# Kernel tuning notes

Measured on AMD Instinct MI355X. Metric: run time of the kernel, lower is better.

## Reference

```python
import jax, jax.numpy as jnp
import numpy as np


def setup_inputs() -> dict:
    key = jax.random.key(0)
    ks = jax.random.split(key, 5)
    B, N, D = 32, 128, 4096
    return {
        "curr_head": jax.random.normal(ks[0], (B, D), jnp.float32),
        "curr_errors": jax.random.normal(ks[1], (B, N, D), jnp.float32),
        "curr_head_2": jax.random.normal(ks[2], (B, D), jnp.float32),
        "curr_errors_2": jax.random.normal(ks[3], (B, N, D), jnp.float32),
        "adv_errors": jax.random.normal(ks[4], (B, N, D), jnp.float32),
        "shared_errors": 128,
    }


def reference(curr_head, curr_errors, curr_head_2, curr_errors_2, adv_errors, shared_errors):
    B = curr_head.shape[0]
    tail = curr_head.shape[1:]
    # (B, N, *tail) -> (N, B, *tail), matching torch's view + transpose(1, 0)
    e1 = jnp.moveaxis(curr_errors.reshape(B, -1, *tail), 1, 0)
    e2 = jnp.moveaxis(curr_errors_2.reshape(B, -1, *tail), 1, 0)
    N1, N2 = e1.shape[0], e2.shape[0]
    s = int(shared_errors)

    def zeros(n):
        return jnp.zeros((n, B) + tail, e1.dtype)

    # self_errors / factor_errors: (N1 + N2 - s, B, *tail)
    self_errors = jnp.concatenate([e1, zeros(N2 - s)], axis=0)
    factor_errors = jnp.concatenate([e2[:s], zeros(N1 - s), e2[s:]], axis=0)

    lin_err = curr_head[None] * factor_errors + curr_head_2[None] * self_errors
    quadr_const = self_errors * factor_errors

    # Exact identity: 0.5*sum_ij |a_i a_j + a_j a_i| = (sum_i |a_i|)^2 (elementwise),
    # since a_i*a_j is already symmetric. Avoids the (N,N,B,*tail) outer product.
    abs_sum = jnp.abs(self_errors).sum(axis=0)
    quadr_error = abs_sum * abs_sum - 0.5 * jnp.abs(quadr_const).sum(axis=0)

    new_head = curr_head * curr_head_2 + 0.5 * quadr_const.sum(axis=0)

    errors = jnp.moveaxis(lin_err, 0, 1)  # (B, N1+N2-s, *tail)
    new_errors = jnp.concatenate([errors, quadr_error[:, None] * adv_errors], axis=1)
    new_errors = new_errors.reshape(-1, *tail)
    return new_head, new_errors
```

## Files before the change

### kernel.cpp

```cpp
#include <hip/hip_runtime.h>

constexpr int B  = 32;
constexpr int N  = 128;
constexpr int D  = 4096;
constexpr int DV = D / 4;
constexpr int COLS   = 64;
constexpr int CHUNKS = 16;
constexpr int NPC    = N / CHUNKS;
constexpr int TPB    = COLS * CHUNKS;
constexpr int TILES  = DV / COLS;

__device__ __forceinline__ float4 f4add(float4 a, float4 b) {
    return make_float4(a.x + b.x, a.y + b.y, a.z + b.z, a.w + b.w);
}

__global__ __launch_bounds__(TPB) void relaxed_prod_kernel(
    const float* __restrict__ h1,
    const float* __restrict__ e1,
    const float* __restrict__ h2,
    const float* __restrict__ e2,
    const float* __restrict__ adv,
    float* __restrict__ out)
{
    const int lane  = threadIdx.x & (COLS - 1);
    const int chunk = threadIdx.x / COLS;
    const int tile  = blockIdx.x % TILES;
    const int b     = blockIdx.x / TILES;
    const int col   = tile * COLS + lane;
    const long d0   = (long)col * 4;

    const float4* e1p  = (const float4*)(e1  + (long)b * N * D + d0);
    const float4* e2p  = (const float4*)(e2  + (long)b * N * D + d0);
    const float4* advp = (const float4*)(adv + (long)b * N * D + d0);
    float4* lin_out = (float4*)(out + (long)B * D + (long)b * (2 * N) * D + d0);
    float4* adv_out = lin_out + (long)N * DV;

    const float4 vh1 = *(const float4*)(h1 + (long)b * D + d0);
    const float4 vh2 = *(const float4*)(h2 + (long)b * D + d0);

    float4 sq  = make_float4(0.f, 0.f, 0.f, 0.f);
    float4 sa  = make_float4(0.f, 0.f, 0.f, 0.f);
    float4 saq = make_float4(0.f, 0.f, 0.f, 0.f);

    const int n0 = chunk * NPC;
#pragma unroll
    for (int i = 0; i < NPC; ++i) {
        const long off = (long)(n0 + i) * DV;
        float4 a = e1p[off];
        float4 c = e2p[off];
        float4 lin;
        lin.x = vh1.x * c.x + vh2.x * a.x;
        lin.y = vh1.y * c.y + vh2.y * a.y;
        lin.z = vh1.z * c.z + vh2.z * a.z;
        lin.w = vh1.w * c.w + vh2.w * a.w;
        lin_out[off] = lin;
        float4 q = make_float4(a.x * c.x, a.y * c.y, a.z * c.z, a.w * c.w);
        sq  = f4add(sq, q);
        sa.x += fabsf(a.x); sa.y += fabsf(a.y); sa.z += fabsf(a.z); sa.w += fabsf(a.w);
        saq.x += fabsf(q.x); saq.y += fabsf(q.y); saq.z += fabsf(q.z); saq.w += fabsf(q.w);
    }

    __shared__ float4 s_q [CHUNKS][COLS];
    __shared__ float4 s_a [CHUNKS][COLS];
    __shared__ float4 s_aq[CHUNKS][COLS];
    __shared__ float4 s_qe[COLS];
    s_q [chunk][lane] = sq;
    s_a [chunk][lane] = sa;
    s_aq[chunk][lane] = saq;
    __syncthreads();

    if (chunk == 0) {
        float4 tq  = s_q [0][lane];
        float4 ta  = s_a [0][lane];
        float4 taq = s_aq[0][lane];
#pragma unroll
        for (int c = 1; c < CHUNKS; ++c) {
            tq  = f4add(tq,  s_q [c][lane]);
            ta  = f4add(ta,  s_a [c][lane]);
            taq = f4add(taq, s_aq[c][lane]);
        }
        float4 qe;
        qe.x = ta.x * ta.x - 0.5f * taq.x;
        qe.y = ta.y * ta.y - 0.5f * taq.y;
        qe.z = ta.z * ta.z - 0.5f * taq.z;
        qe.w = ta.w * ta.w - 0.5f * taq.w;
        float4 nh;
        nh.x = vh1.x * vh2.x + 0.5f * tq.x;
        nh.y = vh1.y * vh2.y + 0.5f * tq.y;
        nh.z = vh1.z * vh2.z + 0.5f * tq.z;
        nh.w = vh1.w * vh2.w + 0.5f * tq.w;
        *(float4*)(out + (long)b * D + d0) = nh;
        s_qe[lane] = qe;
    }
    __syncthreads();

    const float4 qe = s_qe[lane];
#pragma unroll
    for (int i = 0; i < NPC; ++i) {
        const long off = (long)(n0 + i) * DV;
        float4 v = advp[off];
        float4 r = make_float4(qe.x * v.x, qe.y * v.y, qe.z * v.z, qe.w * v.w);
        adv_out[off] = r;
    }
}

extern "C" void kernel_launch(void* const* d_in, const int* in_sizes, int n_in,
                              void* d_out, int out_size, void* d_ws, size_t ws_size,
                              hipStream_t stream) {
    const float* h1  = (const float*)d_in[0];
    const float* e1  = (const float*)d_in[1];
    const float* h2  = (const float*)d_in[2];
    const float* e2  = (const float*)d_in[3];
    const float* adv = (const float*)d_in[4];
    float* out = (float*)d_out;

    dim3 grid(B * TILES);
    dim3 block(TPB);
    relaxed_prod_kernel<<<grid, block, 0, stream>>>(h1, e1, h2, e2, adv, out);
}
```

Baseline: 288.7 us.

## Split fused kernel into three-stage pipeline with global workspace reduction

Replaces the single fused kernel with three launches. The first streams e1/e2 per batch slab and writes partial sums to the workspace, the second reduces the partials to produce new_head and qe, and the third scales adv by qe. Each thread now owns a full 4096-wide row, and rows are split into slabs across blocks. The aim is to drop the intra-block shared-memory barrier and to give longer contiguous streams per block. The cost is extra kernel launches, workspace traffic, and only B*8=256 blocks in the main kernels. The old fused kernel is kept as a fallback when the workspace is too small.

```diff
diff --git a/kernel.cpp b/kernel.cpp
--- a/kernel.cpp
+++ b/kernel.cpp
@@ -4,117 +4,217 @@
 constexpr int N  = 128;
 constexpr int D  = 4096;
 constexpr int DV = D / 4;
-constexpr int COLS   = 64;
-constexpr int CHUNKS = 16;
-constexpr int NPC    = N / CHUNKS;
-constexpr int TPB    = COLS * CHUNKS;
-constexpr int TILES  = DV / COLS;
 
 __device__ __forceinline__ float4 f4add(float4 a, float4 b) {
     return make_float4(a.x + b.x, a.y + b.y, a.z + b.z, a.w + b.w);
 }
-
-__global__ __launch_bounds__(TPB) void relaxed_prod_kernel(
-    const float* __restrict__ h1,
-    const float* __restrict__ e1,
-    const float* __restrict__ h2,
-    const float* __restrict__ e2,
-    const float* __restrict__ adv,
-    float* __restrict__ out)
-{
-    const int lane  = threadIdx.x & (COLS - 1);
-    const int chunk = threadIdx.x / COLS;
-    const int tile  = blockIdx.x % TILES;
-    const int b     = blockIdx.x / TILES;
-    const int col   = tile * COLS + lane;
-    const long d0   = (long)col * 4;
+__device__ __forceinline__ float4 f4mul(float4 a, float4 b) {
+    return make_float4(a.x * b.x, a.y * b.y, a.z * b.z, a.w * b.w);
+}
+__device__ __forceinline__ float4 f4abs(float4 a) {
+    return make_float4(fabsf(a.x), fabsf(a.y), fabsf(a.z), fabsf(a.w));
+}
+
+template <int SLABS>
+__global__ __launch_bounds__(1024) void k_lin_partial(
+    const float4* __restrict__ h1, const float4* __restrict__ e1,
+    const float4* __restrict__ h2, const float4* __restrict__ e2,
+    float4* __restrict__ out, float4* __restrict__ ws)
+{
+    constexpr int R = N / SLABS;
+    const int c    = threadIdx.x;
+    const int slab = blockIdx.x % SLABS;
+    const int b    = blockIdx.x / SLABS;
+    const int n0   = slab * R;
+
+    const float4* e1p = e1 + ((long)b * N + n0) * DV + c;
+    const float4* e2p = e2 + ((long)b * N + n0) * DV + c;
+    float4* linp = out + (long)B * DV + ((long)b * 2 * N + n0) * DV + c;
+
+    const float4 vh1 = h1[(long)b * DV + c];
+    const float4 vh2 = h2[(long)b * DV + c];
+
+    float4 sq  = make_float4(0.f, 0.f, 0.f, 0.f);
+    float4 sa  = make_float4(0.f, 0.f, 0.f, 0.f);
+    float4 saq = make_float4(0.f, 0.f, 0.f, 0.f);
+
+#pragma unroll 4
+    for (int i = 0; i < R; ++i) {
+        float4 a = e1p[(long)i * DV];
+        float4 f = e2p[(long)i * DV];
+        float4 lin;
+        lin.x = vh1.x * f.x + vh2.x * a.x;
+        lin.y = vh1.y * f.y + vh2.y * a.y;
+        lin.z = vh1.z * f.z + vh2.z * a.z;
+        lin.w = vh1.w * f.w + vh2.w * a.w;
+        linp[(long)i * DV] = lin;
+        float4 q = f4mul(a, f);
+        sq  = f4add(sq, q);
+        sa  = f4add(sa, f4abs(a));
+        saq = f4add(saq, f4abs(q));
+    }
+
+    const long pbase = ((long)b * SLABS + slab) * DV + c;
+    const long asz   = (long)B * SLABS * DV;
+    ws[pbase]           = sq;
+    ws[asz + pbase]     = sa;
+    ws[2 * asz + pbase] = saq;
+}
+
+__global__ __launch_bounds__(256) void k_finalize(
+    const float4* __restrict__ h1, const float4* __restrict__ h2,
+    float4* __restrict__ out, float4* __restrict__ ws, int slabs)
+{
+    const int id = blockIdx.x * 256 + threadIdx.x;
+    const int b  = id / DV;
+    const int c  = id % DV;
+    const long asz = (long)B * slabs * DV;
+
+    float4 tq  = make_float4(0.f, 0.f, 0.f, 0.f);
+    float4 ta  = make_float4(0.f, 0.f, 0.f, 0.f);
+    float4 taq = make_float4(0.f, 0.f, 0.f, 0.f);
+    for (int s = 0; s < slabs; ++s) {
+        const long p = ((long)b * slabs + s) * DV + c;
+        tq  = f4add(tq,  ws[p]);
+        ta  = f4add(ta,  ws[asz + p]);
+        taq = f4add(taq, ws[2 * asz + p]);
+    }
+    const float4 vh1 = h1[id];
+    const float4 vh2 = h2[id];
+    float4 nh, qe;
+    nh.x = vh1.x * vh2.x + 0.5f * tq.x;
+    nh.y = vh1.y * vh2.y + 0.5f * tq.y;
+    nh.z = vh1.z * vh2.z + 0.5f * tq.z;
+    nh.w = vh1.w * vh2.w + 0.5f * tq.w;
+    qe.x = ta.x * ta.x - 0.5f * taq.x;
+    qe.y = ta.y * ta.y - 0.5f * taq.y;
+    qe.z = ta.z * ta.z - 0.5f * taq.z;
+    qe.w = ta.w * ta.w - 0.5f * taq.w;
+    out[id] = nh;
+    ws[3 * asz + id] = qe;
+}
+
+template <int SLABS>
+__global__ __launch_bounds__(1024) void k_adv(
+    const float4* __restrict__ adv, float4* __restrict__ out,
+    const float4* __restrict__ ws)
+{
+    constexpr int R = N / SLABS;
+    const int c    = threadIdx.x;
+    const int slab = blockIdx.x % SLABS;
+    const int b    = blockIdx.x / SLABS;
+    const int n0   = slab * R;
+
+    const float4 qe = ws[3L * B * SLABS * DV + (long)b * DV + c];
+    const float4* ap = adv + ((long)b * N + n0) * DV + c;
+    float4* op = out + (long)B * DV + ((long)b * 2 * N + N + n0) * DV + c;
+
+#pragma unroll 4
+    for (int i = 0; i < R; ++i) {
+        float4 v = ap[(long)i * DV];
+        op[(long)i * DV] = f4mul(qe, v);
+    }
+}
+
+constexpr int FB_COLS = 64, FB_CHUNKS = 16, FB_NPC = N / FB_CHUNKS,
+              FB_TPB = FB_COLS * FB_CHUNKS, FB_TILES = DV / FB_COLS;
+
+__global__ __launch_bounds__(FB_TPB) void relaxed_prod_fallback(
+    const float* __restrict__ h1, const float* __restrict__ e1,
+    const float* __restrict__ h2, const float* __restrict__ e2,
+    const float* __restrict__ adv, float* __restrict__ out)
+{
+    const int lane  = threadIdx.x & (FB_COLS - 1);
+    const int chunk = threadIdx.x / FB_COLS;
+    const int tile  = blockIdx.x % FB_TILES;
+    const int b     = blockIdx.x / FB_TILES;
+    const long d0   = ((long)tile * FB_COLS + lane) * 4;
 
     const float4* e1p  = (const float4*)(e1  + (long)b * N * D + d0);
     const float4* e2p  = (const float4*)(e2  + (long)b * N * D + d0);
     const float4* advp = (const float4*)(adv + (long)b * N * D + d0);
     float4* lin_out = (float4*)(out + (long)B * D + (long)b * (2 * N) * D + d0);
     float4* adv_out = lin_out + (long)N * DV;
-
     const float4 vh1 = *(const float4*)(h1 + (long)b * D + d0);
     const float4 vh2 = *(const float4*)(h2 + (long)b * D + d0);
 
-    float4 sq  = make_float4(0.f, 0.f, 0.f, 0.f);
-    float4 sa  = make_float4(0.f, 0.f, 0.f, 0.f);
-    float4 saq = make_float4(0.f, 0.f, 0.f, 0.f);
-
-    const int n0 = chunk * NPC;
+    float4 sq = make_float4(0,0,0,0), sa = make_float4(0,0,0,0), saq = make_float4(0,0,0,0);
+    const int n0 = chunk * FB_NPC;
 #pragma unroll
-    for (int i = 0; i < NPC; ++i) {
+    for (int i = 0; i < FB_NPC; ++i) {
         const long off = (long)(n0 + i) * DV;
-        float4 a = e1p[off];
-        float4 c = e2p[off];
+        float4 a = e1p[off], f = e2p[off];
         float4 lin;
-        lin.x = vh1.x * c.x + vh2.x * a.x;
-        lin.y = vh1.y * c.y + vh2.y * a.y;
-        lin.z = vh1.z * c.z + vh2.z * a.z;
-        lin.w = vh1.w * c.w + vh2.w * a.w;
+        lin.x = vh1.x * f.x + vh2.x * a.x; lin.y = vh1.y * f.y + vh2.y * a.y;
+        lin.z = vh1.z * f.z + vh2.z * a.z; lin.w = vh1.w * f.w + vh2.w * a.w;
         lin_out[off] = lin;
-        float4 q = make_float4(a.x * c.x, a.y * c.y, a.z * c.z, a.w * c.w);
-        sq  = f4add(sq, q);
-        sa.x += fabsf(a.x); sa.y += fabsf(a.y); sa.z += fabsf(a.z); sa.w += fabsf(a.w);
-        saq.x += fabsf(q.x); saq.y += fabsf(q.y); saq.z += fabsf(q.z); saq.w += fabsf(q.w);
-    }
-
-    __shared__ float4 s_q [CHUNKS][COLS];
-    __shared__ float4 s_a [CHUNKS][COLS];
-    __shared__ float4 s_aq[CHUNKS][COLS];
-    __shared__ float4 s_qe[COLS];
-    s_q [chunk][lane] = sq;
-    s_a [chunk][lane] = sa;
-    s_aq[chunk][lane] = saq;
+        float4 q = f4mul(a, f);
+        sq = f4add(sq, q); sa = f4add(sa, f4abs(a)); saq = f4add(saq, f4abs(q));
+    }
+    __shared__ float4 s_q[FB_CHUNKS][FB_COLS], s_a[FB_CHUNKS][FB_COLS],
+                      s_aq[FB_CHUNKS][FB_COLS], s_qe[FB_COLS];
+    s_q[chunk][lane] = sq; s_a[chunk][lane] = sa; s_aq[chunk][lane] = saq;
     __syncthreads();
-
     if (chunk == 0) {
-        float4 tq  = s_q [0][lane];
-        float4 ta  = s_a [0][lane];
-        float4 taq = s_aq[0][lane];
+        float4 tq = s_q[0][lane], ta = s_a[0][lane], taq = s_aq[0][lane];
 #pragma unroll
-        for (int c = 1; c < CHUNKS; ++c) {
-            tq  = f4add(tq,  s_q [c][lane]);
-            ta  = f4add(ta,  s_a [c][lane]);
-            taq = f4add(taq, s_aq[c][lane]);
+        for (int cc = 1; cc < FB_CHUNKS; ++cc) {
+            tq = f4add(tq, s_q[cc][lane]); ta = f4add(ta, s_a[cc][lane]);
+            taq = f4add(taq, s_aq[cc][lane]);
         }
-        float4 qe;
-        qe.x = ta.x * ta.x - 0.5f * taq.x;
-        qe.y = ta.y * ta.y - 0.5f * taq.y;
-        qe.z = ta.z * ta.z - 0.5f * taq.z;
-        qe.w = ta.w * ta.w - 0.5f * taq.w;
-        float4 nh;
-        nh.x = vh1.x * vh2.x + 0.5f * tq.x;
-        nh.y = vh1.y * vh2.y + 0.5f * tq.y;
-        nh.z = vh1.z * vh2.z + 0.5f * tq.z;
-        nh.w = vh1.w * vh2.w + 0.5f * tq.w;
+        float4 qe, nh;
+        qe.x = ta.x * ta.x - 0.5f * taq.x; qe.y = ta.y * ta.y - 0.5f * taq.y;
+        qe.z = ta.z * ta.z - 0.5f * taq.z; qe.w = ta.w * ta.w - 0.5f * taq.w;
+        nh.x = vh1.x * vh2.x + 0.5f * tq.x; nh.y = vh1.y * vh2.y + 0.5f * tq.y;
+        nh.z = vh1.z * vh2.z + 0.5f * tq.z; nh.w = vh1.w * vh2.w + 0.5f * tq.w;
         *(float4*)(out + (long)b * D + d0) = nh;
         s_qe[lane] = qe;
     }
     __syncthreads();
-
     const float4 qe = s_qe[lane];
 #pragma unroll
-    for (int i = 0; i < NPC; ++i) {
+    for (int i = 0; i < FB_NPC; ++i) {
         const long off = (long)(n0 + i) * DV;
-        float4 v = advp[off];
-        float4 r = make_float4(qe.x * v.x, qe.y * v.y, qe.z * v.z, qe.w * v.w);
-        adv_out[off] = r;
-    }
+        adv_out[off] = f4mul(qe, advp[off]);
+    }
+}
+
+template <int SLABS>
+static void launch_pipeline(const float4* h1, const float4* e1,
+                            const float4* h2, const float4* e2,
+                            const float4* adv, float4* out, float4* ws,
+                            hipStream_t stream)
+{
+    k_lin_partial<SLABS><<<dim3(B * SLABS), dim3(1024), 0, stream>>>(h1, e1, h2, e2, out, ws);
+    k_finalize<<<dim3(B * DV / 256), dim3(256), 0, stream>>>(h1, h2, out, ws, SLABS);
+    k_adv<SLABS><<<dim3(B * SLABS), dim3(1024), 0, stream>>>(adv, out, ws);
 }
 
 extern "C" void kernel_launch(void* const* d_in, const int* in_sizes, int n_in,
                               void* d_out, int out_size, void* d_ws, size_t ws_size,
                               hipStream_t stream) {
-    const float* h1  = (const float*)d_in[0];
-    const float* e1  = (const float*)d_in[1];
-    const float* h2  = (const float*)d_in[2];
-    const float* e2  = (const float*)d_in[3];
-    const float* adv = (const float*)d_in[4];
-    float* out = (float*)d_out;
-
-    dim3 grid(B * TILES);
-    dim3 block(TPB);
-    relaxed_prod_kernel<<<grid, block, 0, stream>>>(h1, e1, h2, e2, adv, out);
-}
+    const float4* h1  = (const float4*)d_in[0];
+    const float4* e1  = (const float4*)d_in[1];
+    const float4* h2  = (const float4*)d_in[2];
+    const float4* e2  = (const float4*)d_in[3];
+    const float4* adv = (const float4*)d_in[4];
+    float4* out = (float4*)d_out;
+    float4* ws  = (float4*)d_ws;
+
+    auto need = [](int slabs) -> size_t {
+        return ((size_t)3 * B * slabs * DV + (size_t)B * DV) * sizeof(float4);
+    };
+    if (ws_size >= need(8)) {
+        launch_pipeline<8>(h1, e1, h2, e2, adv, out, ws, stream);
+    } else if (ws_size >= need(4)) {
+        launch_pipeline<4>(h1, e1, h2, e2, adv, out, ws, stream);
+    } else if (ws_size >= need(2)) {
+        launch_pipeline<2>(h1, e1, h2, e2, adv, out, ws, stream);
+    } else if (ws_size >= need(1)) {
+        launch_pipeline<1>(h1, e1, h2, e2, adv, out, ws, stream);
+    } else {
+        relaxed_prod_fallback<<<dim3(B * FB_TILES), dim3(FB_TPB), 0, stream>>>(
+            (const float*)d_in[0], (const float*)d_in[1], (const float*)d_in[2],
+            (const float*)d_in[3], (const float*)d_in[4], (float*)d_out);
+    }
+}
```

Result: slower. 301.7 us (+4.5%).
